# Kernel optimization log

Measured on AMD Instinct MI355X. Metric: run time of the kernel, lower is better.

## Reference

```python
import math
import jax, jax.numpy as jnp
import numpy as np

FS = 16000          # sample rate implied by undefined global `fs` in source
NFFT = 320          # win_len == frame_len
HOP = 160           # inc
C_SOUND = 340.0
ARRAY_DIS = 0.027


def _steering(F, n_ch, angle_deg):
    # h = conj(exp(-1j*2*pi*f_k * sensor * d * sin(theta)/c)) -> exp(+1j*...)
    f_k = np.arange(F) * (FS // NFFT)                      # integer bins * 50 Hz
    delay = np.arange(n_ch) * ARRAY_DIS * np.sin(angle_deg * np.pi / 180.0) / C_SOUND
    h = np.exp(1j * 2.0 * np.pi * f_k[:, None] * delay[None, :]).astype(np.complex64)
    return jnp.asarray(h)[..., None]                       # [F, C, 1]


def _stft(x, window):
    # x: [B, C, L] float32; torch.stft defaults: center=True, reflect pad
    pad = NFFT // 2
    xp = jnp.pad(x, ((0, 0), (0, 0), (pad, pad)), mode='reflect')
    T = 1 + (xp.shape[-1] - NFFT) // HOP
    idx = jnp.arange(T)[:, None] * HOP + jnp.arange(NFFT)[None, :]
    frames = xp[:, :, idx] * window                        # [B, C, T, NFFT]
    return jnp.fft.rfft(frames, axis=-1)                   # [B, C, T, F] complex64


def _istft(S):
    # S: [B, F, T] complex; torch.istft with default (rectangular) window
    frames = jnp.fft.irfft(jnp.moveaxis(S, 1, 2), n=NFFT, axis=-1)  # [B, T, NFFT]
    B, T, _ = frames.shape
    out_len = NFFT + HOP * (T - 1)
    idx = jnp.arange(T)[:, None] * HOP + jnp.arange(NFFT)[None, :]
    out = jnp.zeros((B, out_len), frames.dtype).at[:, idx].add(frames)
    wsum = jnp.zeros((out_len,), frames.dtype).at[idx.reshape(-1)].add(1.0)
    pad = NFFT // 2
    return (out / wsum)[:, pad:-pad]


def setup_inputs() -> dict:
    key = jax.random.key(0)
    B, L, C = 8, 160000, 4
    mc_wav = jax.random.normal(key, (B, L, C), dtype=jnp.float32)
    # torch.kaiser_window(320, periodic=True, beta=6)
    window = jnp.asarray(np.kaiser(NFFT + 1, 6.0)[:NFFT].astype(np.float32))
    return {"mc_wav": mc_wav, "window": window}


def reference(mc_wav, window):
    B, L, C = mc_wav.shape
    # pre-normalize: remove DC per channel, scale by per-batch global max-abs
    x = mc_wav - jnp.mean(mc_wav, axis=1, keepdims=True)
    x = x / jnp.max(jnp.abs(x), axis=(1, 2), keepdims=True)
    x = jnp.transpose(x, (0, 2, 1))                        # [B, C, L]

    S = _stft(x, window)                                   # [B, C, T, F]
    F = S.shape[-1]
    Xs = jnp.transpose(S, (2, 0, 3, 1))                    # [T, B, F, C] frames-first
    T = Xs.shape[0]

    h1 = _steering(F, C, -40.0)                            # [F, C, 1]
    h2 = _steering(F, C, 40.0)
    eye = jnp.eye(C, dtype=S.dtype)

    def beam(invR, h, X):
        num = jnp.einsum('bfcd,fdo->bfco', invR, h)        # invR @ h  [B,F,C,1]
        den = jnp.einsum('fco,bfco->bf', h.conj(), num)    # h^H invR h
        w = num[..., 0] / den[..., None]                   # [B, F, C]
        return jnp.einsum('bfc,bfc->bf', w.conj(), X)      # w^H X

    def step(RXX, inp):
        X, first = inp                                     # X: [B, F, C]
        outer = jnp.einsum('bfc,bfd->bfcd', X, X.conj())
        RXX = jnp.where(first, outer, 0.05 * RXX + 0.95 * outer)
        tr = jnp.trace(RXX, axis1=-2, axis2=-1)[..., None, None]
        invR = jnp.linalg.inv(RXX + (tr / C) * eye)        # diag-loaded inverse
        return RXX, (beam(invR, h1, X), beam(invR, h2, X))

    RXX0 = jnp.zeros((B, F, C, C), dtype=S.dtype)
    firsts = jnp.arange(T) == 0
    _, (s1, s2) = jax.lax.scan(step, RXX0, (Xs, firsts))

    S1 = jnp.transpose(s1, (1, 2, 0))                      # [B, F, T]
    S2 = jnp.transpose(s2, (1, 2, 0))
    return _istft(S1), _istft(S2)
```

## Files before the change

kernel.cpp:

```cpp
#include <hip/hip_runtime.h>
#include <hip/hip_bf16.h>
#include <math.h>

#define BB 8
#define LL 160000
#define CC 4
#define NFFT 320
#define HOP 160
#define FB 161
#define TT 1001
#define TP 1024
#define RBLK 128
#define PI_D 3.14159265358979323846
#define NPAD 160320

#define CH 2
#define SCH 504
#define KWARM 4

#define GM 16016
#define KSEC 352
#define LDK 704
#define KT 11

typedef __attribute__((ext_vector_type(8))) short bf16x8;
typedef __attribute__((ext_vector_type(4))) float f32x4;

__device__ __forceinline__ void ldsdma16(const short* g, short* l){
    __builtin_amdgcn_global_load_lds((const __attribute__((address_space(1))) void*)g,
                                     (__attribute__((address_space(3))) void*)l, 16, 0, 0);
}

__device__ __forceinline__ float2 cmulf(float2 a, float2 b){
    return make_float2(a.x*b.x - a.y*b.y, a.x*b.y + a.y*b.x);
}
__device__ __forceinline__ float2 cmulcj(float2 a, float2 b){
    return make_float2(a.x*b.x + a.y*b.y, a.y*b.x - a.x*b.y);
}
__device__ __forceinline__ float2 cjmul(float2 a, float2 b){
    return make_float2(a.x*b.x + a.y*b.y, a.x*b.y - a.y*b.x);
}
__device__ __forceinline__ float2 csub(float2 a, float2 b){ return make_float2(a.x-b.x, a.y-b.y); }
__device__ __forceinline__ float2 cscale(float2 a, float s){ return make_float2(a.x*s, a.y*s); }
__device__ __forceinline__ float2 cdivf(float2 a, float2 b){
    float inv = 1.0f/(b.x*b.x + b.y*b.y);
    return make_float2((a.x*b.x + a.y*b.y)*inv, (a.y*b.x - a.x*b.y)*inv);
}
__device__ __forceinline__ short bf_hi(float v){
    __hip_bfloat16 h = __float2bfloat16(v);
    short s; __builtin_memcpy(&s, &h, 2); return s;
}
__device__ __forceinline__ short bf_lo(float v){
    __hip_bfloat16 h = __float2bfloat16(v);
    float r = v - __bfloat162float(h);
    __hip_bfloat16 l = __float2bfloat16(r);
    short s; __builtin_memcpy(&s, &l, 2); return s;
}

__global__ void k_gen(const float* __restrict__ win, float* __restrict__ htab,
                      short* __restrict__ Bts, short* __restrict__ Bt){
    int gid = blockIdx.x*256 + threadIdx.x;
    if (gid < 2*FB*CC){
        int i = gid;
        int c = i & 3;
        int k = (i >> 2) % FB;
        int m = i / (FB*CC);
        double coef = 2.0*PI_D*50.0*0.027*sin(40.0*PI_D/180.0)/340.0;
        double sgn = (m == 0) ? -1.0 : 1.0;
        double ph = sgn*coef*(double)k*(double)c;
        double s, c2;
        sincos(ph, &s, &c2);
        ((float2*)htab)[i] = make_float2((float)c2, (float)s);
        return;
    }
    gid -= 2*FB*CC;
    if (gid < 384*640){
        int col = gid / 640, kk = gid % 640;
        int n = (kk >= 320) ? kk - 320 : kk;
        int sec = (kk >= 320) ? 1 : 0;
        float v = 0.f;
        if (col < 2*FB){
            int k = col >> 1;
            double th = 2.0*PI_D*(double)k*(double)n/320.0;
            double s, co; sincos(th, &s, &co);
            double tw = (col & 1) ? -s : co;
            v = (float)((double)win[n]*tw);
        }
        Bts[gid] = sec ? bf_lo(v) : bf_hi(v);
        return;
    }
    gid -= 384*640;
    if (gid < NFFT*LDK){
        int n = gid / LDK, kk = gid % LDK;
        int sec = (kk >= KSEC) ? 1 : 0;
        int kk2 = kk - (sec ? KSEC : 0);
        float v = 0.f;
        if (kk2 < 2*FB){
            int bin = kk2 >> 1;
            double c = ((bin == 0 || bin == 160) ? 1.0 : 2.0) / 320.0;
            double th = 2.0*PI_D*(double)bin*(double)n/320.0;
            double s, co; sincos(th, &s, &co);
            v = (float)((kk2 & 1) ? -c*s : c*co);
        }
        Bt[(size_t)n*LDK + kk] = sec ? bf_lo(v) : bf_hi(v);
    }
}

__global__ __launch_bounds__(256) void k_stats1(const float* __restrict__ in, float* __restrict__ part){
    __shared__ float4 s4[256];
    __shared__ float4 mn4[256];
    __shared__ float4 mx4[256];
    int b = blockIdx.x / RBLK, chunk = blockIdx.x % RBLK;
    int tid = threadIdx.x;
    const float4* p = (const float4*)(in + (size_t)b*LL*CC);
    const int per = LL / RBLK;
    int start = chunk*per;
    float4 s  = make_float4(0.f,0.f,0.f,0.f);
    float4 mn = make_float4( 3.4e38f, 3.4e38f, 3.4e38f, 3.4e38f);
    float4 mx = make_float4(-3.4e38f,-3.4e38f,-3.4e38f,-3.4e38f);
    for (int i = start + tid; i < start + per; i += 256){
        float4 v = p[i];
        s.x += v.x; s.y += v.y; s.z += v.z; s.w += v.w;
        mn.x = fminf(mn.x, v.x); mn.y = fminf(mn.y, v.y); mn.z = fminf(mn.z, v.z); mn.w = fminf(mn.w, v.w);
        mx.x = fmaxf(mx.x, v.x); mx.y = fmaxf(mx.y, v.y); mx.z = fmaxf(mx.z, v.z); mx.w = fmaxf(mx.w, v.w);
    }
    s4[tid] = s; mn4[tid] = mn; mx4[tid] = mx;
    __syncthreads();
    for (int st = 128; st >= 1; st >>= 1){
        if (tid < st){
            float4 a = s4[tid], c = s4[tid+st];
            s4[tid] = make_float4(a.x+c.x, a.y+c.y, a.z+c.z, a.w+c.w);
            float4 d = mn4[tid], e = mn4[tid+st];
            mn4[tid] = make_float4(fminf(d.x,e.x), fminf(d.y,e.y), fminf(d.z,e.z), fminf(d.w,e.w));
            float4 f = mx4[tid], g = mx4[tid+st];
            mx4[tid] = make_float4(fmaxf(f.x,g.x), fmaxf(f.y,g.y), fmaxf(f.z,g.z), fmaxf(f.w,g.w));
        }
        __syncthreads();
    }
    if (tid == 0){
        float* dst = part + (size_t)(b*RBLK + chunk)*12;
        float4 a = s4[0], d = mn4[0], f = mx4[0];
        dst[0]=a.x; dst[1]=a.y; dst[2]=a.z; dst[3]=a.w;
        dst[4]=d.x; dst[5]=d.y; dst[6]=d.z; dst[7]=d.w;
        dst[8]=f.x; dst[9]=f.y; dst[10]=f.z; dst[11]=f.w;
    }
}

__global__ __launch_bounds__(128) void k_stats2(const float* __restrict__ part,
                                                float* __restrict__ mean, float* __restrict__ invmax){
    __shared__ float4 s4[128];
    __shared__ float4 mn4[128];
    __shared__ float4 mx4[128];
    int b = blockIdx.x, tid = threadIdx.x;
    const float* src = part + (size_t)(b*RBLK + tid)*12;
    s4[tid]  = make_float4(src[0], src[1], src[2], src[3]);
    mn4[tid] = make_float4(src[4], src[5], src[6], src[7]);
    mx4[tid] = make_float4(src[8], src[9], src[10], src[11]);
    __syncthreads();
    for (int st = 64; st >= 1; st >>= 1){
        if (tid < st){
            float4 a = s4[tid], c = s4[tid+st];
            s4[tid] = make_float4(a.x+c.x, a.y+c.y, a.z+c.z, a.w+c.w);
            float4 d = mn4[tid], e = mn4[tid+st];
            mn4[tid] = make_float4(fminf(d.x,e.x), fminf(d.y,e.y), fminf(d.z,e.z), fminf(d.w,e.w));
            float4 f = mx4[tid], g = mx4[tid+st];
            mx4[tid] = make_float4(fmaxf(f.x,g.x), fmaxf(f.y,g.y), fmaxf(f.z,g.z), fmaxf(f.w,g.w));
        }
        __syncthreads();
    }
    if (tid == 0){
        float4 sum = s4[0], mn = mn4[0], mx = mx4[0];
        float m0 = sum.x*(1.0f/LL), m1 = sum.y*(1.0f/LL), m2 = sum.z*(1.0f/LL), m3 = sum.w*(1.0f/LL);
        mean[b*4+0]=m0; mean[b*4+1]=m1; mean[b*4+2]=m2; mean[b*4+3]=m3;
        float a0 = fmaxf(mx.x - m0, m0 - mn.x);
        float a1 = fmaxf(mx.y - m1, m1 - mn.y);
        float a2 = fmaxf(mx.z - m2, m2 - mn.z);
        float a3 = fmaxf(mx.w - m3, m3 - mn.w);
        invmax[b] = 1.0f / fmaxf(fmaxf(a0, a1), fmaxf(a2, a3));
    }
}

__global__ __launch_bounds__(256) void k_anorm(const float* __restrict__ in,
        const float* __restrict__ mean, const float* __restrict__ invmax,
        short* __restrict__ Ahi, short* __restrict__ Alo){
    int gid = blockIdx.x*256 + threadIdx.x;
    if (gid >= BB*CC*(NPAD/8)) return;
    int p8 = gid % (NPAD/8);
    int bc = gid / (NPAD/8);
    int b = bc >> 2;
    float mc = mean[bc];
    float iv = invmax[b];
    const float* px = in + (size_t)b*LL*CC + (bc & 3);
    bf16x8 h8, l8;
    #pragma unroll
    for (int j = 0; j < 8; ++j){
        int p = p8*8 + j - 160;
        int m2 = p < 0 ? -p : (p >= LL ? 2*LL - 2 - p : p);
        float v = (px[(size_t)m2*CC] - mc) * iv;
        __hip_bfloat16 h = __float2bfloat16(v);
        float r = v - __bfloat162float(h);
        __hip_bfloat16 l = __float2bfloat16(r);
        short hs, ls; __builtin_memcpy(&hs, &h, 2); __builtin_memcpy(&ls, &l, 2);
        h8[j] = hs; l8[j] = ls;
    }
    size_t o = (size_t)bc*NPAD + (size_t)p8*8;
    *(bf16x8*)&Ahi[o] = h8;
    *(bf16x8*)&Alo[o] = l8;
}

__global__ __launch_bounds__(256) void k_gstft(const short* __restrict__ Ahi, const short* __restrict__ Alo,
        const short* __restrict__ Bts, float* __restrict__ S){
    __shared__ short stage[16384];
    float* Ct = (float*)stage;
    int tid = threadIdx.x;
    int row0 = blockIdx.x*64;
    int col0 = blockIdx.y*64;
    int b  = row0 >> 12;
    int t0 = (row0 & 4095) >> 2;
    if (t0 >= TT) return;
    int wave = tid >> 6, lane = tid & 63;
    int wm = wave >> 1, wn = wave & 1;
    int l15 = lane & 15, quad = lane >> 4;
    int rowS  = wave*16 + (lane >> 2);
    int chunk = (lane & 3) ^ ((lane >> 3) & 3);
    int tls = t0 + (rowS >> 2); if (tls >= TT) tls = TT - 1;
    size_t gao = (size_t)(b*4 + (rowS & 3))*NPAD + (size_t)tls*160 + chunk*8;
    const short* gAh = Ahi + gao;
    const short* gAl = Alo + gao;
    const short* gB  = Bts + (size_t)(col0 + rowS)*640 + chunk*8;
    short* lA = stage + wave*512;
    int sw  = (l15 >> 1) & 3;
    int c0r = (quad ^ sw) * 8;
    int ra0 = (wm*32 + l15)*32 + c0r;
    int ra1 = (wm*32 + 16 + l15)*32 + c0r;
    int rb0 = (wn*32 + l15)*32 + c0r;
    int rb1 = (wn*32 + 16 + l15)*32 + c0r;
    f32x4 acc00 = {0.f,0.f,0.f,0.f}, acc01 = acc00, acc10 = acc00, acc11 = acc00;

    #define STG(kt_, off_) do{ \
        ldsdma16(gAh + (kt_)*32,       lA + (off_));        \
        ldsdma16(gAl + (kt_)*32,       lA + (off_) + 2048); \
        ldsdma16(gB  + (kt_)*32,       lA + (off_) + 4096); \
        ldsdma16(gB  + (kt_)*32 + 320, lA + (off_) + 6144); \
    }while(0)

    STG(0, 0);
    __syncthreads();
    int offc = 0;
    #pragma unroll
    for (int kt = 0; kt < 10; ++kt){
        int offn = 8192 - offc;
        if (kt < 9) STG(kt+1, offn);
        bf16x8 a0h = *(bf16x8*)&stage[offc + ra0];
        bf16x8 a1h = *(bf16x8*)&stage[offc + ra1];
        bf16x8 a0l = *(bf16x8*)&stage[offc + 2048 + ra0];
        bf16x8 a1l = *(bf16x8*)&stage[offc + 2048 + ra1];
        bf16x8 b0h = *(bf16x8*)&stage[offc + 4096 + rb0];
        bf16x8 b1h = *(bf16x8*)&stage[offc + 4096 + rb1];
        bf16x8 b0l = *(bf16x8*)&stage[offc + 6144 + rb0];
        bf16x8 b1l = *(bf16x8*)&stage[offc + 6144 + rb1];
        acc00 = __builtin_amdgcn_mfma_f32_16x16x32_bf16(a0h, b0h, acc00, 0, 0, 0);
        acc01 = __builtin_amdgcn_mfma_f32_16x16x32_bf16(a0h, b1h, acc01, 0, 0, 0);
        acc10 = __builtin_amdgcn_mfma_f32_16x16x32_bf16(a1h, b0h, acc10, 0, 0, 0);
        acc11 = __builtin_amdgcn_mfma_f32_16x16x32_bf16(a1h, b1h, acc11, 0, 0, 0);
        acc00 = __builtin_amdgcn_mfma_f32_16x16x32_bf16(a0l, b0h, acc00, 0, 0, 0);
        acc01 = __builtin_amdgcn_mfma_f32_16x16x32_bf16(a0l, b1h, acc01, 0, 0, 0);
        acc10 = __builtin_amdgcn_mfma_f32_16x16x32_bf16(a1l, b0h, acc10, 0, 0, 0);
        acc11 = __builtin_amdgcn_mfma_f32_16x16x32_bf16(a1l, b1h, acc11, 0, 0, 0);
        acc00 = __builtin_amdgcn_mfma_f32_16x16x32_bf16(a0h, b0l, acc00, 0, 0, 0);
        acc01 = __builtin_amdgcn_mfma_f32_16x16x32_bf16(a0h, b1l, acc01, 0, 0, 0);
        acc10 = __builtin_amdgcn_mfma_f32_16x16x32_bf16(a1h, b0l, acc10, 0, 0, 0);
        acc11 = __builtin_amdgcn_mfma_f32_16x16x32_bf16(a1h, b1l, acc11, 0, 0, 0);
        __syncthreads();
        offc = offn;
    }
    #undef STG
    #pragma unroll
    for (int r = 0; r < 4; ++r){
        int rl = wm*32 + quad*4 + r;
        Ct[rl*66 + wn*32 + l15]           = acc00[r];
        Ct[rl*66 + wn*32 + l15 + 16]      = acc01[r];
        Ct[(rl+16)*66 + wn*32 + l15]      = acc10[r];
        Ct[(rl+16)*66 + wn*32 + l15 + 16] = acc11[r];
    }
    __syncthreads();
    int tl = tid & 15, h = (tid >> 4) & 1, kq = tid >> 5;
    int t = t0 + tl;
    if (t < TT){
        float4* S4 = (float4*)S;
        for (int kk = kq; kk < 32; kk += 8){
            int kg = (col0 >> 1) + kk;
            if (kg < FB){
                float2 e0 = *(float2*)&Ct[(tl*4 + 2*h)*66 + 2*kk];
                float2 e1 = *(float2*)&Ct[(tl*4 + 2*h + 1)*66 + 2*kk];
                S4[((size_t)(b*FB + kg)*TT + t)*2 + h] = make_float4(e0.x, e0.y, e1.x, e1.y);
            }
        }
    }
}

#define UPD(first) do{ \
    float aa = (first) ? 0.f : 0.05f; float wg = (first) ? 1.f : 0.95f; \
    float y0x=wg*x0.x, y0y=wg*x0.y, y1x=wg*x1.x, y1y=wg*x1.y; \
    float y2x=wg*x2.x, y2y=wg*x2.y, y3x=wg*x3.x, y3y=wg*x3.y; \
    d0 = aa*d0 + y0x*x0.x + y0y*x0.y; \
    d1 = aa*d1 + y1x*x1.x + y1y*x1.y; \
    d2 = aa*d2 + y2x*x2.x + y2y*x2.y; \
    d3 = aa*d3 + y3x*x3.x + y3y*x3.y; \
    r10.x = aa*r10.x + y1x*x0.x + y1y*x0.y;  r10.y = aa*r10.y + y1y*x0.x - y1x*x0.y; \
    r20.x = aa*r20.x + y2x*x0.x + y2y*x0.y;  r20.y = aa*r20.y + y2y*x0.x - y2x*x0.y; \
    r30.x = aa*r30.x + y3x*x0.x + y3y*x0.y;  r30.y = aa*r30.y + y3y*x0.x - y3x*x0.y; \
    r21.x = aa*r21.x + y2x*x1.x + y2y*x1.y;  r21.y = aa*r21.y + y2y*x1.x - y2x*x1.y; \
    r31.x = aa*r31.x + y3x*x1.x + y3y*x1.y;  r31.y = aa*r31.y + y3y*x1.x - y3x*x1.y; \
    r32.x = aa*r32.x + y3x*x2.x + y3y*x2.y;  r32.y = aa*r32.y + y3y*x2.x - y3x*x2.y; \
}while(0)

__global__ __launch_bounds__(256) void k_scan(const float* __restrict__ S, const float* __restrict__ htab,
                      float* __restrict__ S1, float* __restrict__ S2){
    __shared__ float4 tile[1008];
    int bid = blockIdx.x;
    int half = bid & 1;
    int bf = bid >> 1;
    int f  = bf % FB;
    int tid = threadIdx.x;
    int tbase = half*SCH;
    int te  = tbase + SCH; if (te > TT) te = TT;
    int nst = 2*(te - tbase);
    const float4* Sg = (const float4*)S + (size_t)bf*TT*2;
    const float4* Sp = Sg + (size_t)tbase*2;
    for (int i = tid; i < nst; i += 256)
        tile[i ^ ((i>>4)&7)] = Sp[i];
    __syncthreads();
    float2 out1[CH], out2[CH];
    int t0 = tbase + tid*CH;
    bool act = (tid*CH < SCH) && (t0 < TT);
    if (act){
        const float2* hp = (const float2*)htab;
        float2 ha0 = hp[f*4+0], ha1 = hp[f*4+1], ha2 = hp[f*4+2], ha3 = hp[f*4+3];
        float2 hb0 = hp[(FB+f)*4+0], hb1 = hp[(FB+f)*4+1], hb2 = hp[(FB+f)*4+2], hb3 = hp[(FB+f)*4+3];
        float d0=0,d1=0,d2=0,d3=0;
        float2 r10={0,0}, r20={0,0}, r30={0,0}, r21={0,0}, r31={0,0}, r32={0,0};
        int ts = t0 - KWARM; if (ts < 0) ts = 0;
        for (int tau = ts; tau < t0; ++tau){
            float4 v0, v1;
            if (tau >= tbase){
                int i0 = 2*(tau - tbase);
                v0 = tile[i0 ^ ((i0>>4)&7)];
                v1 = tile[(i0+1) ^ ((i0>>4)&7)];
            } else {
                v0 = Sg[2*tau];
                v1 = Sg[2*tau + 1];
            }
            float2 x0 = make_float2(v0.x, v0.y), x1 = make_float2(v0.z, v0.w);
            float2 x2 = make_float2(v1.x, v1.y), x3 = make_float2(v1.z, v1.w);
            UPD(tau == 0);
        }
        for (int j = 0; j < CH; ++j){
            int t = t0 + j;
            if (t >= TT) break;
            int i0 = 2*(t - tbase);
            float4 v0 = tile[i0 ^ ((i0>>4)&7)];
            float4 v1 = tile[(i0+1) ^ ((i0>>4)&7)];
            float2 x0 = make_float2(v0.x, v0.y), x1 = make_float2(v0.z, v0.w);
            float2 x2 = make_float2(v1.x, v1.y), x3 = make_float2(v1.z, v1.w);
            UPD(t == 0);
            float trc = d0 + d1 + d2 + d3;
            float lam = trc * 0.25f;
            float e0 = d0 + lam, e1 = d1 + lam, e2 = d2 + lam, e3 = d3 + lam;
            float detP = e0*e1 - (r10.x*r10.x + r10.y*r10.y);
            float2 w00 = csub(cscale(r20, e1), cmulf(r10, r21));
            float2 w01 = csub(cscale(r30, e1), cmulf(r10, r31));
            float2 w10 = csub(cscale(r21, e0), cjmul(r10, r20));
            float2 w11 = csub(cscale(r31, e0), cjmul(r10, r30));
            float2 va = cjmul(r30, w00), vb = cjmul(r31, w10);
            float2 V10 = make_float2(va.x + vb.x, -(va.y + vb.y));
            float reV00 = r20.x*w00.x + r20.y*w00.y + r21.x*w10.x + r21.y*w10.y;
            float reV11 = r30.x*w01.x + r30.y*w01.y + r31.x*w11.x + r31.y*w11.y;
            float t00 = detP*e2 - reV00;
            float t11 = detP*e3 - reV11;
            float2 t10 = csub(cscale(r32, detP), V10);
            float detT = t00*t11 - (t10.x*t10.x + t10.y*t10.y);
            #pragma unroll
            for (int m = 0; m < 2; ++m){
                float2 h0 = m ? hb0 : ha0;
                float2 h1 = m ? hb1 : ha1;
                float2 h2 = m ? hb2 : ha2;
                float2 h3 = m ? hb3 : ha3;
                float2 g0 = csub(cscale(h0, e1), cjmul(r10, h1));
                float2 g1 = csub(cscale(h1, e0), cmulf(r10, h0));
                float2 ta = cmulf(r20, g0), tb = cmulf(r21, g1);
                float2 hh0 = make_float2(detP*h2.x - ta.x - tb.x, detP*h2.y - ta.y - tb.y);
                ta = cmulf(r30, g0); tb = cmulf(r31, g1);
                float2 hh1 = make_float2(detP*h3.x - ta.x - tb.x, detP*h3.y - ta.y - tb.y);
                float2 y20 = csub(cscale(hh0, t11), cjmul(t10, hh1));
                float2 y21 = csub(cscale(hh1, t00), cmulf(t10, hh0));
                float2 u20 = cscale(y20, detP), u21 = cscale(y21, detP);
                ta = cmulcj(y20, r20); tb = cmulcj(y21, r30);
                float2 q0 = make_float2(detT*h0.x - ta.x - tb.x, detT*h0.y - ta.y - tb.y);
                ta = cmulcj(y20, r21); tb = cmulcj(y21, r31);
                float2 q1 = make_float2(detT*h1.x - ta.x - tb.x, detT*h1.y - ta.y - tb.y);
                float2 u10 = csub(cscale(q0, e1), cjmul(r10, q1));
                float2 u11 = csub(cscale(q1, e0), cmulf(r10, q0));
                float2 den = cjmul(h0, u10), tmp;
                tmp = cjmul(h1, u11); den.x += tmp.x; den.y += tmp.y;
                tmp = cjmul(h2, u20); den.x += tmp.x; den.y += tmp.y;
                tmp = cjmul(h3, u21); den.x += tmp.x; den.y += tmp.y;
                float2 num = cjmul(u10, x0);
                tmp = cjmul(u11, x1); num.x += tmp.x; num.y += tmp.y;
                tmp = cjmul(u20, x2); num.x += tmp.x; num.y += tmp.y;
                tmp = cjmul(u21, x3); num.x += tmp.x; num.y += tmp.y;
                float2 s = cdivf(num, make_float2(den.x, -den.y));
                if (m) out2[j] = s; else out1[j] = s;
            }
        }
    }
    __syncthreads();
    float2* o1 = (float2*)tile;
    float2* o2 = ((float2*)tile) + 528;
    if (act){
        for (int j = 0; j < CH && t0 + j < TT; ++j){
            int lt = t0 - tbase + j;
            int iw = lt ^ ((lt>>3)&7);
            o1[iw] = out1[j];
            o2[iw] = out2[j];
        }
    }
    __syncthreads();
    int nout = te - tbase;
    float2* S1g = (float2*)S1 + (size_t)bf*TT + tbase;
    float2* S2g = (float2*)S2 + (size_t)bf*TT + tbase;
    for (int i = tid; i < nout; i += 256){
        int ir = i ^ ((i>>3)&7);
        S1g[i] = o1[ir];
        S2g[i] = o2[ir];
    }
}

__global__ __launch_bounds__(256) void k_pack(const float* __restrict__ S1, const float* __restrict__ S2,
                                              short* __restrict__ A){
    __shared__ short tile[32*708];
    int bid = blockIdx.x;
    int tb = bid & 31, rb = bid >> 5;
    int t0 = tb*32;
    int beam = rb >> 3, b = rb & 7;
    const float2* Sp = (const float2*)(beam ? S2 : S1) + (size_t)b*FB*TT;
    int tid = threadIdx.x;
    for (int idx = tid; idx < 32*176; idx += 256){
        int bin = idx >> 5, tq = idx & 31;
        int t = t0 + tq;
        float2 s = make_float2(0.f, 0.f);
        if (bin < FB && t < TT) s = Sp[(size_t)bin*TT + t];
        int c0 = 2*bin;
        tile[tq*708 + c0]            = bf_hi(s.x);
        tile[tq*708 + c0 + 1]        = bf_hi(s.y);
        tile[tq*708 + KSEC + c0]     = bf_lo(s.x);
        tile[tq*708 + KSEC + c0 + 1] = bf_lo(s.y);
    }
    __syncthreads();
    for (int idx = tid; idx < 32*176; idx += 256){
        int tq = idx / 176, k4 = idx % 176;
        int t = t0 + tq;
        if (t < TT)
            *(short4*)&A[(size_t)(rb*TT + t)*LDK + k4*4] = *(short4*)&tile[tq*708 + k4*4];
    }
}

__global__ __launch_bounds__(256) void k_gemm(const short* __restrict__ A, const short* __restrict__ Bt,
                                              float* __restrict__ C){
    __shared__ short sb2[8192];
    int tid = threadIdx.x;
    int row0 = blockIdx.x * 64;
    int col0 = blockIdx.y * 64;
    int wave = tid >> 6, lane = tid & 63;
    int wm = wave >> 1, wn = wave & 1;
    int l15 = lane & 15, quad = lane >> 4;
    int rowS  = wave*16 + (lane >> 2);
    int chunk = (lane & 3) ^ ((lane >> 3) & 3);
    int grS = row0 + rowS; if (grS >= GM) grS = GM - 1;
    const short* gA = A  + (size_t)grS*LDK + chunk*8;
    const short* gB = Bt + (size_t)(col0 + rowS)*LDK + chunk*8;
    short* lA = sb2 + wave*512;
    int sw  = (l15 >> 1) & 3;
    int c0r = (quad ^ sw) * 8;
    int ra0 = (wm*32 + l15)*32 + c0r;
    int ra1 = (wm*32 + 16 + l15)*32 + c0r;
    int rb0 = (wn*32 + l15)*32 + c0r;
    int rb1 = (wn*32 + 16 + l15)*32 + c0r;
    f32x4 acc00 = {0.f,0.f,0.f,0.f}, acc01 = acc00, acc10 = acc00, acc11 = acc00;

    #define KOF(s_, ka_, kb_) { int sg_ = ((s_) >= 22) ? 2 : ((s_) >= 11) ? 1 : 0; \
        int kt_ = (s_) - sg_*11; \
        ka_ = ((sg_ == 1) ? KSEC : 0) + kt_*32; \
        kb_ = ((sg_ == 2) ? KSEC : 0) + kt_*32; }
    #define STG2(s_, off_) do{ int ka_, kb_; KOF(s_, ka_, kb_); \
        ldsdma16(gA + ka_, lA + (off_));        \
        ldsdma16(gB + kb_, lA + (off_) + 2048); \
    }while(0)

    STG2(0, 0);
    __syncthreads();
    int offc = 0;
    #pragma unroll
    for (int s = 0; s < 33; ++s){
        int offn = 4096 - offc;
        if (s < 32) STG2(s+1, offn);
        bf16x8 a0 = *(bf16x8*)&sb2[offc + ra0];
        bf16x8 a1 = *(bf16x8*)&sb2[offc + ra1];
        bf16x8 b0 = *(bf16x8*)&sb2[offc + 2048 + rb0];
        bf16x8 b1 = *(bf16x8*)&sb2[offc + 2048 + rb1];
        acc00 = __builtin_amdgcn_mfma_f32_16x16x32_bf16(a0, b0, acc00, 0, 0, 0);
        acc01 = __builtin_amdgcn_mfma_f32_16x16x32_bf16(a0, b1, acc01, 0, 0, 0);
        acc10 = __builtin_amdgcn_mfma_f32_16x16x32_bf16(a1, b0, acc10, 0, 0, 0);
        acc11 = __builtin_amdgcn_mfma_f32_16x16x32_bf16(a1, b1, acc11, 0, 0, 0);
        __syncthreads();
        offc = offn;
    }
    #undef STG2
    #undef KOF
    for (int r = 0; r < 4; ++r){
        int orow0 = row0 + wm*32 + quad*4 + r;
        int ocol0 = col0 + wn*32 + l15;
        if (orow0 < GM){
            C[(size_t)orow0*NFFT + ocol0]      = acc00[r];
            C[(size_t)orow0*NFFT + ocol0 + 16] = acc01[r];
        }
        if (orow0 + 16 < GM){
            C[(size_t)(orow0+16)*NFFT + ocol0]      = acc10[r];
            C[(size_t)(orow0+16)*NFFT + ocol0 + 16] = acc11[r];
        }
    }
}

__global__ __launch_bounds__(256) void k_ola(const float* __restrict__ frames, float* __restrict__ out){
    int gid = blockIdx.x*256 + threadIdx.x;
    if (gid >= 2*BB*(LL/4)) return;
    int o4 = (gid % (LL/4))*4;
    int rb = gid / (LL/4);
    int i  = o4 + HOP;
    int t1 = i / HOP;
    int r  = i - t1*HOP;
    const float4* fb = (const float4*)(frames + (size_t)rb*TT*NFFT);
    float4 a = fb[(t1*NFFT + r) >> 2];
    float4 b = fb[((t1-1)*NFFT + r + HOP) >> 2];
    ((float4*)out)[gid] = make_float4(0.5f*(a.x+b.x), 0.5f*(a.y+b.y), 0.5f*(a.z+b.z), 0.5f*(a.w+b.w));
}

extern "C" void kernel_launch(void* const* d_in, const int* in_sizes, int n_in,
                              void* d_out, int out_size, void* d_ws, size_t ws_size,
                              hipStream_t stream){
    const float* in  = (const float*)d_in[0];
    const float* win = (const float*)d_in[1];
    float* ws = (float*)d_ws;
    float* mean   = ws;
    float* invmax = ws + 32;
    float* htab   = ws + 48;
    float* S1     = ws + 3072;
    size_t nS1 = (size_t)2*BB*FB*TT;
    float* S2 = S1 + nS1;
    float* S  = S2 + nS1;
    float* part = S1;
    short* Ahi = (short*)S1;
    short* Alo = Ahi + (size_t)BB*CC*NPAD;
    short* Bts = (short*)d_out;
    short* Bt  = (short*)((float*)d_out + 131072);
    short* A  = (short*)S;
    float* frames = S1;

    int ngen = 2*FB*CC + 384*640 + NFFT*LDK;
    k_gen<<<dim3((ngen + 255)/256), dim3(256), 0, stream>>>(win, htab, Bts, Bt);
    k_stats1<<<dim3(BB*RBLK), dim3(256), 0, stream>>>(in, part);
    k_stats2<<<dim3(BB), dim3(128), 0, stream>>>(part, mean, invmax);
    k_anorm<<<dim3((BB*CC*(NPAD/8) + 255)/256), dim3(256), 0, stream>>>(in, mean, invmax, Ahi, Alo);
    k_gstft<<<dim3(BB*TP*CC/64, 6), dim3(256), 0, stream>>>(Ahi, Alo, Bts, S);
    k_scan<<<dim3(2*BB*FB), dim3(256), 0, stream>>>(S, htab, S1, S2);
    k_pack<<<dim3(512), dim3(256), 0, stream>>>(S1, S2, A);
    k_gemm<<<dim3((GM + 63)/64, NFFT/64), dim3(256), 0, stream>>>(A, Bt, frames);
    k_ola<<<dim3((2*BB*(LL/4) + 255)/256), dim3(256), 0, stream>>>(frames, (float*)d_out);
}
```

Before: 220.8 us.

## Prefetch two stages ahead in GEMMs and give scan one timestep per thread

```diff
diff --git a/kernel.cpp b/kernel.cpp
--- a/kernel.cpp
+++ b/kernel.cpp
@@ -14,7 +14,6 @@
 #define PI_D 3.14159265358979323846
 #define NPAD 160320
 
-#define CH 2
 #define SCH 504
 #define KWARM 4
 
@@ -245,12 +244,13 @@
     }while(0)
 
     STG(0, 0);
-    __syncthreads();
-    int offc = 0;
+    STG(1, 8192);
     #pragma unroll
     for (int kt = 0; kt < 10; ++kt){
-        int offn = 8192 - offc;
-        if (kt < 9) STG(kt+1, offn);
+        int offc = (kt & 1) ? 8192 : 0;
+        if (kt < 9) asm volatile("s_waitcnt vmcnt(4)" ::: "memory");
+        else        asm volatile("s_waitcnt vmcnt(0)" ::: "memory");
+        __builtin_amdgcn_s_barrier();
         bf16x8 a0h = *(bf16x8*)&stage[offc + ra0];
         bf16x8 a1h = *(bf16x8*)&stage[offc + ra1];
         bf16x8 a0l = *(bf16x8*)&stage[offc + 2048 + ra0];
@@ -259,6 +259,10 @@
         bf16x8 b1h = *(bf16x8*)&stage[offc + 4096 + rb1];
         bf16x8 b0l = *(bf16x8*)&stage[offc + 6144 + rb0];
         bf16x8 b1l = *(bf16x8*)&stage[offc + 6144 + rb1];
+        asm volatile("s_waitcnt lgkmcnt(0)" ::: "memory");
+        __builtin_amdgcn_sched_barrier(0);
+        __builtin_amdgcn_s_barrier();
+        if (kt < 8) STG(kt+2, offc);
         acc00 = __builtin_amdgcn_mfma_f32_16x16x32_bf16(a0h, b0h, acc00, 0, 0, 0);
         acc01 = __builtin_amdgcn_mfma_f32_16x16x32_bf16(a0h, b1h, acc01, 0, 0, 0);
         acc10 = __builtin_amdgcn_mfma_f32_16x16x32_bf16(a1h, b0h, acc10, 0, 0, 0);
@@ -271,8 +275,6 @@
         acc01 = __builtin_amdgcn_mfma_f32_16x16x32_bf16(a0h, b1l, acc01, 0, 0, 0);
         acc10 = __builtin_amdgcn_mfma_f32_16x16x32_bf16(a1h, b0l, acc10, 0, 0, 0);
         acc11 = __builtin_amdgcn_mfma_f32_16x16x32_bf16(a1h, b1l, acc11, 0, 0, 0);
-        __syncthreads();
-        offc = offn;
     }
     #undef STG
     #pragma unroll
@@ -315,7 +317,7 @@
     r32.x = aa*r32.x + y3x*x2.x + y3y*x2.y;  r32.y = aa*r32.y + y3y*x2.x - y3x*x2.y; \
 }while(0)
 
-__global__ __launch_bounds__(256) void k_scan(const float* __restrict__ S, const float* __restrict__ htab,
+__global__ __launch_bounds__(512) void k_scan(const float* __restrict__ S, const float* __restrict__ htab,
                       float* __restrict__ S1, float* __restrict__ S2){
     __shared__ float4 tile[1008];
     int bid = blockIdx.x;
@@ -328,12 +330,12 @@
     int nst = 2*(te - tbase);
     const float4* Sg = (const float4*)S + (size_t)bf*TT*2;
     const float4* Sp = Sg + (size_t)tbase*2;
-    for (int i = tid; i < nst; i += 256)
+    for (int i = tid; i < nst; i += 512)
         tile[i ^ ((i>>4)&7)] = Sp[i];
     __syncthreads();
-    float2 out1[CH], out2[CH];
-    int t0 = tbase + tid*CH;
-    bool act = (tid*CH < SCH) && (t0 < TT);
+    float2 out1, out2;
+    int t0 = tbase + tid;
+    bool act = (tid < SCH) && (t0 < TT);
     if (act){
         const float2* hp = (const float2*)htab;
         float2 ha0 = hp[f*4+0], ha1 = hp[f*4+1], ha2 = hp[f*4+2], ha3 = hp[f*4+3];
@@ -355,9 +357,8 @@
             float2 x2 = make_float2(v1.x, v1.y), x3 = make_float2(v1.z, v1.w);
             UPD(tau == 0);
         }
-        for (int j = 0; j < CH; ++j){
-            int t = t0 + j;
-            if (t >= TT) break;
+        {
+            int t = t0;
             int i0 = 2*(t - tbase);
             float4 v0 = tile[i0 ^ ((i0>>4)&7)];
             float4 v1 = tile[(i0+1) ^ ((i0>>4)&7)];
@@ -410,7 +411,7 @@
                 tmp = cjmul(u20, x2); num.x += tmp.x; num.y += tmp.y;
                 tmp = cjmul(u21, x3); num.x += tmp.x; num.y += tmp.y;
                 float2 s = cdivf(num, make_float2(den.x, -den.y));
-                if (m) out2[j] = s; else out1[j] = s;
+                if (m) out2 = s; else out1 = s;
             }
         }
     }
@@ -418,18 +419,16 @@
     float2* o1 = (float2*)tile;
     float2* o2 = ((float2*)tile) + 528;
     if (act){
-        for (int j = 0; j < CH && t0 + j < TT; ++j){
-            int lt = t0 - tbase + j;
-            int iw = lt ^ ((lt>>3)&7);
-            o1[iw] = out1[j];
-            o2[iw] = out2[j];
-        }
+        int lt = t0 - tbase;
+        int iw = lt ^ ((lt>>3)&7);
+        o1[iw] = out1;
+        o2[iw] = out2;
     }
     __syncthreads();
     int nout = te - tbase;
     float2* S1g = (float2*)S1 + (size_t)bf*TT + tbase;
     float2* S2g = (float2*)S2 + (size_t)bf*TT + tbase;
-    for (int i = tid; i < nout; i += 256){
+    for (int i = tid; i < nout; i += 512){
         int ir = i ^ ((i>>3)&7);
         S1g[i] = o1[ir];
         S2g[i] = o2[ir];
@@ -498,22 +497,25 @@
     }while(0)
 
     STG2(0, 0);
-    __syncthreads();
-    int offc = 0;
+    STG2(1, 4096);
     #pragma unroll
     for (int s = 0; s < 33; ++s){
-        int offn = 4096 - offc;
-        if (s < 32) STG2(s+1, offn);
+        int offc = (s & 1) ? 4096 : 0;
+        if (s < 32) asm volatile("s_waitcnt vmcnt(2)" ::: "memory");
+        else        asm volatile("s_waitcnt vmcnt(0)" ::: "memory");
+        __builtin_amdgcn_s_barrier();
         bf16x8 a0 = *(bf16x8*)&sb2[offc + ra0];
         bf16x8 a1 = *(bf16x8*)&sb2[offc + ra1];
         bf16x8 b0 = *(bf16x8*)&sb2[offc + 2048 + rb0];
         bf16x8 b1 = *(bf16x8*)&sb2[offc + 2048 + rb1];
+        asm volatile("s_waitcnt lgkmcnt(0)" ::: "memory");
+        __builtin_amdgcn_sched_barrier(0);
+        __builtin_amdgcn_s_barrier();
+        if (s < 31) STG2(s+2, offc);
         acc00 = __builtin_amdgcn_mfma_f32_16x16x32_bf16(a0, b0, acc00, 0, 0, 0);
         acc01 = __builtin_amdgcn_mfma_f32_16x16x32_bf16(a0, b1, acc01, 0, 0, 0);
         acc10 = __builtin_amdgcn_mfma_f32_16x16x32_bf16(a1, b0, acc10, 0, 0, 0);
         acc11 = __builtin_amdgcn_mfma_f32_16x16x32_bf16(a1, b1, acc11, 0, 0, 0);
-        __syncthreads();
-        offc = offn;
     }
     #undef STG2
     #undef KOF
@@ -572,7 +574,7 @@
     k_stats2<<<dim3(BB), dim3(128), 0, stream>>>(part, mean, invmax);
     k_anorm<<<dim3((BB*CC*(NPAD/8) + 255)/256), dim3(256), 0, stream>>>(in, mean, invmax, Ahi, Alo);
     k_gstft<<<dim3(BB*TP*CC/64, 6), dim3(256), 0, stream>>>(Ahi, Alo, Bts, S);
-    k_scan<<<dim3(2*BB*FB), dim3(256), 0, stream>>>(S, htab, S1, S2);
+    k_scan<<<dim3(2*BB*FB), dim3(512), 0, stream>>>(S, htab, S1, S2);
     k_pack<<<dim3(512), dim3(256), 0, stream>>>(S1, S2, A);
     k_gemm<<<dim3((GM + 63)/64, NFFT/64), dim3(256), 0, stream>>>(A, Bt, frames);
     k_ola<<<dim3((2*BB*(LL/4) + 255)/256), dim3(256), 0, stream>>>(frames, (float*)d_out);
```

Measured after the change: 220.4 us. No clear change (-0.2%).
